# Kernel optimization log

Measured on AMD Instinct MI355X. Metric: run time of the kernel, lower is better.

## Reference

```python
import jax, jax.numpy as jnp
import numpy as np
import math

B, S, IN_DIM = 2048, 60, 211
D, H, L, DFF, NC = 192, 6, 3, 768, 35
DK = D // H


def make_pe(seq_len, d_model):
    pos = np.arange(seq_len)[:, None].astype(np.float32)
    div = np.exp(np.arange(0, d_model, 2).astype(np.float32) * (-math.log(10000.0) / d_model))
    pe = np.zeros((seq_len, d_model), dtype=np.float32)
    pe[:, 0::2] = np.sin(pos * div)
    pe[:, 1::2] = np.cos(pos * div)
    return jnp.asarray(pe)


def setup_inputs() -> dict:
    key = jax.random.key(0)
    ks = jax.random.split(key, 24)
    r = lambda k, shape, fan: jax.random.normal(k, shape, jnp.float32) * (1.0 / np.sqrt(fan))
    inp = {
        'x': jax.random.normal(ks[0], (B, S, IN_DIM), jnp.float32),
        'W_in': r(ks[1], (IN_DIM, D), IN_DIM), 'b_in': jnp.zeros((D,), jnp.float32),
        'pe': make_pe(S, D),
        'Wq': r(ks[2], (L, D, D), D), 'bq': jnp.zeros((L, D), jnp.float32),
        'Wk': r(ks[3], (L, D, D), D), 'bk': jnp.zeros((L, D), jnp.float32),
        'Wv': r(ks[4], (L, D, D), D), 'bv': jnp.zeros((L, D), jnp.float32),
        'Wo': r(ks[5], (L, D, D), D), 'bo': jnp.zeros((L, D), jnp.float32),
        'W1': r(ks[6], (L, D, DFF), D), 'b1': jnp.zeros((L, DFF), jnp.float32),
        'W2': r(ks[7], (L, DFF, D), DFF), 'b2': jnp.zeros((L, D), jnp.float32),
        'g1': jnp.ones((L, D), jnp.float32), 'be1': jnp.zeros((L, D), jnp.float32),
        'g2': jnp.ones((L, D), jnp.float32), 'be2': jnp.zeros((L, D), jnp.float32),
        'Wc1': r(ks[8], (D, D // 2), D), 'bc1': jnp.zeros((D // 2,), jnp.float32),
        'Wc2': r(ks[9], (D // 2, NC), D // 2), 'bc2': jnp.zeros((NC,), jnp.float32),
    }
    return inp


def layer_norm(x, g, b, eps=1e-5):
    mu = jnp.mean(x, axis=-1, keepdims=True)
    var = jnp.mean((x - mu) ** 2, axis=-1, keepdims=True)
    return (x - mu) * jax.lax.rsqrt(var + eps) * g + b


def mha(x, Wq, bq, Wk, bk, Wv, bv, Wo, bo):
    Bs, Ss, _ = x.shape
    q = (x @ Wq + bq).reshape(Bs, Ss, H, DK)
    k = (x @ Wk + bk).reshape(Bs, Ss, H, DK)
    v = (x @ Wv + bv).reshape(Bs, Ss, H, DK)
    scores = jnp.einsum('bqhd,bkhd->bhqk', q, k) / jnp.sqrt(jnp.float32(DK))
    attn = jax.nn.softmax(scores, axis=-1)
    ctx = jnp.einsum('bhqk,bkhd->bqhd', attn, v).reshape(Bs, Ss, D)
    return ctx @ Wo + bo


def encoder_layer(x, Wq, bq, Wk, bk, Wv, bv, Wo, bo, W1, b1, W2, b2, g1, be1, g2, be2):
    attn_out = mha(x, Wq, bq, Wk, bk, Wv, bv, Wo, bo)
    x = layer_norm(x + attn_out, g1, be1)
    ff = jax.nn.gelu(x @ W1 + b1, approximate=False) @ W2 + b2
    return layer_norm(x + ff, g2, be2)


def reference(x, W_in, b_in, pe, Wq, bq, Wk, bk, Wv, bv, Wo, bo,
              W1, b1, W2, b2, g1, be1, g2, be2, Wc1, bc1, Wc2, bc2):
    h = x @ W_in + b_in + pe  # [B,S,D]
    for l in range(L):
        h = encoder_layer(h, Wq[l], bq[l], Wk[l], bk[l], Wv[l], bv[l], Wo[l], bo[l],
                          W1[l], b1[l], W2[l], b2[l], g1[l], be1[l], g2[l], be2[l])
    hidden = jax.nn.gelu(h @ Wc1 + bc1, approximate=False)
    return hidden @ Wc2 + bc2  # [B,S,NC]
```

## Files before the change

kernel.cpp:

```cpp
#include <hip/hip_runtime.h>
#include <cmath>

#define B_   2048
#define S_   60
#define NTOK (B_*S_)
#define IND_ 211
#define D_   192
#define H_   6
#define DK_  32
#define L_   3
#define DFF_ 768
#define NC_  35
#define DH_  96

typedef unsigned short us_t;
typedef us_t us8 __attribute__((ext_vector_type(8)));
typedef us_t us4 __attribute__((ext_vector_type(4)));
typedef short sh8 __attribute__((ext_vector_type(8)));
typedef float f4 __attribute__((ext_vector_type(4)));

#define MFMA(a, b, cc) __builtin_amdgcn_mfma_f32_16x16x32_bf16((a), (b), (cc), 0, 0, 0)
#define ZACC(A, M, N) \
    for (int _i = 0; _i < (M); ++_i) \
        for (int _j = 0; _j < (N); ++_j) { \
            A[_i][_j][0] = 0.f; A[_i][_j][1] = 0.f; A[_i][_j][2] = 0.f; A[_i][_j][3] = 0.f; }
#define ZACC1(A, N) \
    for (int _j = 0; _j < (N); ++_j) { \
        A[_j][0] = 0.f; A[_j][1] = 0.f; A[_j][2] = 0.f; A[_j][3] = 0.f; }

__device__ __forceinline__ float bf2f(us_t u) {
    union { unsigned int i; float f; } v; v.i = ((unsigned int)u) << 16; return v.f;
}
__device__ __forceinline__ us_t f2bf(float f) {
    union { float f; unsigned int i; } v; v.f = f;
    unsigned int r = v.i + 0x7fffu + ((v.i >> 16) & 1u);
    return (us_t)(r >> 16);
}
__device__ __forceinline__ float gelu_f(float v) {
    float u = v * (0.7978845608f + 0.0356774081f * v * v);
    float e = __expf(2.f * u);
    float t = 1.f - 2.f / (e + 1.f);
    return 0.5f * v * (1.f + t);
}
__device__ __forceinline__ void gld16(const us_t* g, us_t* s) {
    __builtin_amdgcn_global_load_lds(
        (const __attribute__((address_space(1))) unsigned int*)(g),
        (__attribute__((address_space(3))) unsigned int*)(s), 16, 0, 0);
}

__global__ void prep_t(const float* __restrict__ in, us_t* __restrict__ out,
                       int K, int Kpad, int N)
{
    int e = blockIdx.x * 256 + threadIdx.x;
    if (e >= N * Kpad) return;
    int n = e / Kpad, kp = e % Kpad;
    out[e] = (kp < K) ? f2bf(in[(size_t)kp * N + n]) : (us_t)0;
}

__global__ void prep_ff(const float* __restrict__ W1, const float* __restrict__ W2,
                        us_t* __restrict__ W1T, us_t* __restrict__ W2T)
{
    int e = blockIdx.x * 256 + threadIdx.x;
    if (e >= L_ * 12 * 13824) return;
    int l = e / (12 * 13824), r = e % (12 * 13824);
    int tile = r / 13824, q = r % 13824;
    int col = q / 72, kk = q % 72;
    int cb = tile / 3, pc = tile % 3;
    us_t v1 = 0, v2 = 0;
    if (kk < 64) {
        v1 = f2bf(W1[((size_t)l * D_ + pc * 64 + kk) * DFF_ + cb * D_ + col]);
        v2 = f2bf(W2[((size_t)l * DFF_ + cb * D_ + pc * 64 + kk) * D_ + col]);
    }
    W1T[e] = v1; W2T[e] = v2;
}

__global__ __launch_bounds__(256) void inp_mfma(
    const float* __restrict__ x, const us_t* __restrict__ Wint,
    const float* __restrict__ b_in, const float* __restrict__ pe,
    us_t* __restrict__ h)
{
    __shared__ __align__(16) char smem[29696 + 27648];
    us_t* Xs = (us_t*)smem;
    us_t* Ws = (us_t*)(smem + 29696);
    const int tid = threadIdx.x;
    const int lane = tid & 63, wid = tid >> 6;
    const int g = lane >> 4, c = lane & 15;
    const int wr = wid >> 1, wc = wid & 1;
    const int row0 = blockIdx.x * 64;

    for (int e = tid; e < 64 * 224; e += 256) {
        int tok = e / 224, kp = e % 224;
        float v = (kp < IND_) ? x[(size_t)(row0 + tok) * IND_ + kp] : 0.f;
        Xs[tok * 232 + kp] = f2bf(v);
    }

    f4 acc[2][6];
    ZACC(acc, 2, 6);
    for (int pc = 0; pc < 4; ++pc) {
        __syncthreads();
        const int nk = (pc < 3) ? 64 : 32;
        const int per = nk / 8;
        for (int e = tid; e < 192 * per; e += 256) {
            int rw = e / per, v = e % per;
            *(us8*)&Ws[rw * 72 + v * 8] =
                *(const us8*)&Wint[(size_t)rw * 224 + pc * 64 + v * 8];
        }
        __syncthreads();
        for (int kk = 0; kk < nk / 32; ++kk) {
            const int ka = pc * 64 + kk * 32 + g * 8;
            const int kw = kk * 32 + g * 8;
            sh8 a0 = *(const sh8*)&Xs[(32 * wr + c) * 232 + ka];
            sh8 a1 = *(const sh8*)&Xs[(32 * wr + 16 + c) * 232 + ka];
            #pragma unroll
            for (int ni = 0; ni < 6; ++ni) {
                sh8 bf = *(const sh8*)&Ws[(96 * wc + 16 * ni + c) * 72 + kw];
                acc[0][ni] = MFMA(a0, bf, acc[0][ni]);
                acc[1][ni] = MFMA(a1, bf, acc[1][ni]);
            }
        }
    }
    #pragma unroll
    for (int ni = 0; ni < 6; ++ni) {
        const int col = 96 * wc + 16 * ni + c;
        const float bv = b_in[col];
        #pragma unroll
        for (int mi = 0; mi < 2; ++mi)
            #pragma unroll
            for (int r = 0; r < 4; ++r) {
                int tokg = row0 + 32 * wr + 16 * mi + 4 * g + r;
                int s = tokg % S_;
                float val = acc[mi][ni][r] + bv + pe[(size_t)s * D_ + col];
                h[(size_t)tokg * D_ + col] = f2bf(val);
            }
    }
}

__global__ __launch_bounds__(1024) void qkv_attn_wo(
    us_t* __restrict__ h,
    const us_t* __restrict__ Wqt, const us_t* __restrict__ Wkt,
    const us_t* __restrict__ Wvt, const us_t* __restrict__ Wot,
    const float* __restrict__ bq, const float* __restrict__ bk,
    const float* __restrict__ bv, const float* __restrict__ bo,
    const float* __restrict__ g1, const float* __restrict__ be1)
{
    __shared__ __align__(16) char smem[157696];
    us_t* Xs  = (us_t*)smem;
    us_t* Qs  = (us_t*)(smem + 25600);
    us_t* Ks  = (us_t*)(smem + 51200);
    us_t* Vt  = (us_t*)(smem + 76800);
    us_t* Ws  = (us_t*)(smem + 104448);
    us_t* Pb3 = (us_t*)(smem + 104448);
    us_t* Cx  = (us_t*)(smem + 132096);
    float* eL = (float*)(smem + 51200);

    const int tid = threadIdx.x;
    const int lane = tid & 63, wid = tid >> 6;
    const int g = lane >> 4, c = lane & 15;
    const int wr = wid >> 2, wc = wid & 3;
    us_t* hb = h + (size_t)blockIdx.x * (S_ * D_);

    for (int e = tid; e < 1536; e += 1024) {
        int tok = e / 24, v = e % 24;
        us8 u = {0, 0, 0, 0, 0, 0, 0, 0};
        if (tok < S_) u = *(const us8*)&hb[(size_t)tok * D_ + v * 8];
        *(us8*)&Xs[tok * 200 + v * 8] = u;
    }

    for (int m = 0; m < 3; ++m) {
        const us_t* Wt = (m == 0) ? Wqt : (m == 1) ? Wkt : Wvt;
        const float* bb = (m == 0) ? bq : (m == 1) ? bk : bv;
        f4 acc[3];
        ZACC1(acc, 3);
        for (int pc = 0; pc < 3; ++pc) {
            __syncthreads();
            for (int e = tid; e < 1536; e += 1024) {
                int rw = e >> 3, v = e & 7;
                *(us8*)&Ws[rw * 72 + v * 8] =
                    *(const us8*)&Wt[(size_t)rw * 192 + pc * 64 + v * 8];
            }
            __syncthreads();
            #pragma unroll
            for (int kk = 0; kk < 2; ++kk) {
                const int ka = pc * 64 + kk * 32 + g * 8;
                const int kw = kk * 32 + g * 8;
                sh8 a0 = *(const sh8*)&Xs[(16 * wr + c) * 200 + ka];
                #pragma unroll
                for (int ni = 0; ni < 3; ++ni) {
                    sh8 bf = *(const sh8*)&Ws[(48 * wc + 16 * ni + c) * 72 + kw];
                    acc[ni] = MFMA(a0, bf, acc[ni]);
                }
            }
        }
        #pragma unroll
        for (int ni = 0; ni < 3; ++ni) {
            const int col = 48 * wc + 16 * ni + c;
            const float bval = bb[col];
            #pragma unroll
            for (int r = 0; r < 4; ++r) {
                int tok = 16 * wr + 4 * g + r;
                us_t o = f2bf(acc[ni][r] + bval);
                if (m == 0)      Qs[tok * 200 + col] = o;
                else if (m == 1) Ks[tok * 200 + col] = o;
                else             Vt[col * 72 + tok] = o;
            }
        }
    }
    __syncthreads();

    for (int rr2 = 0; rr2 < 2; ++rr2) {
        const bool act = (wid < 12);
        const int hh = 3 * rr2 + (wid >> 2);
        const int hgrp = wid & 3;
        us_t* Pb = Pb3 + (size_t)(wid >> 2) * 4608;
        if (act) {
            f4 sc[4];
            ZACC1(sc, 4);
            const int ka = 32 * hh + g * 8;
            sh8 aq = *(const sh8*)&Qs[(16 * hgrp + c) * 200 + ka];
            #pragma unroll
            for (int ni = 0; ni < 4; ++ni) {
                sh8 bk8 = *(const sh8*)&Ks[(16 * ni + c) * 200 + ka];
                sc[ni] = MFMA(aq, bk8, sc[ni]);
            }
            #pragma unroll
            for (int r = 0; r < 4; ++r) {
                float mx = -1e30f;
                #pragma unroll
                for (int ni = 0; ni < 4; ++ni) {
                    float v = sc[ni][r] * 0.17677669529663687f;
                    if (16 * ni + c >= S_) v = -1e30f;
                    sc[ni][r] = v;
                    mx = fmaxf(mx, v);
                }
                mx = fmaxf(mx, __shfl_xor(mx, 1));
                mx = fmaxf(mx, __shfl_xor(mx, 2));
                mx = fmaxf(mx, __shfl_xor(mx, 4));
                mx = fmaxf(mx, __shfl_xor(mx, 8));
                float sum = 0.f;
                #pragma unroll
                for (int ni = 0; ni < 4; ++ni) {
                    float e = __expf(sc[ni][r] - mx);
                    sc[ni][r] = e; sum += e;
                }
                sum += __shfl_xor(sum, 1);
                sum += __shfl_xor(sum, 2);
                sum += __shfl_xor(sum, 4);
                sum += __shfl_xor(sum, 8);
                const float inv = 1.f / sum;
                #pragma unroll
                for (int ni = 0; ni < 4; ++ni)
                    Pb[(16 * hgrp + 4 * g + r) * 72 + 16 * ni + c] = f2bf(sc[ni][r] * inv);
            }
        }
        __syncthreads();
        if (act) {
            f4 ov[2];
            ZACC1(ov, 2);
            #pragma unroll
            for (int kk = 0; kk < 2; ++kk) {
                sh8 ap = *(const sh8*)&Pb[(16 * hgrp + c) * 72 + kk * 32 + g * 8];
                #pragma unroll
                for (int n2 = 0; n2 < 2; ++n2) {
                    sh8 bv8 = *(const sh8*)&Vt[(32 * hh + 16 * n2 + c) * 72 + kk * 32 + g * 8];
                    ov[n2] = MFMA(ap, bv8, ov[n2]);
                }
            }
            #pragma unroll
            for (int n2 = 0; n2 < 2; ++n2)
                #pragma unroll
                for (int r = 0; r < 4; ++r)
                    Cx[(16 * hgrp + 4 * g + r) * 200 + 32 * hh + 16 * n2 + c] = f2bf(ov[n2][r]);
        }
        __syncthreads();
    }

    f4 aw[3];
    ZACC1(aw, 3);
    for (int pc = 0; pc < 3; ++pc) {
        __syncthreads();
        for (int e = tid; e < 1536; e += 1024) {
            int rw = e >> 3, v = e & 7;
            *(us8*)&Ws[rw * 72 + v * 8] =
                *(const us8*)&Wot[(size_t)rw * 192 + pc * 64 + v * 8];
        }
        __syncthreads();
        #pragma unroll
        for (int kk = 0; kk < 2; ++kk) {
            const int ka = pc * 64 + kk * 32 + g * 8;
            const int kw = kk * 32 + g * 8;
            sh8 a0 = *(const sh8*)&Cx[(16 * wr + c) * 200 + ka];
            #pragma unroll
            for (int ni = 0; ni < 3; ++ni) {
                sh8 bf = *(const sh8*)&Ws[(48 * wc + 16 * ni + c) * 72 + kw];
                aw[ni] = MFMA(a0, bf, aw[ni]);
            }
        }
    }
    __syncthreads();
    #pragma unroll
    for (int ni = 0; ni < 3; ++ni) {
        const int col = 48 * wc + 16 * ni + c;
        const float bov = bo[col];
        #pragma unroll
        for (int r = 0; r < 4; ++r) {
            int tok = 16 * wr + 4 * g + r;
            eL[tok * 200 + col] = aw[ni][r] + bov + bf2f(Xs[tok * 200 + col]);
        }
    }
    __syncthreads();
    {
        const int tl = tid >> 4, t16 = tid & 15;
        float vals[12], sum = 0.f, ssq = 0.f;
        #pragma unroll
        for (int jv = 0; jv < 3; ++jv) {
            float4 v4 = *(const float4*)&eL[tl * 200 + t16 * 12 + jv * 4];
            vals[jv*4+0] = v4.x; vals[jv*4+1] = v4.y; vals[jv*4+2] = v4.z; vals[jv*4+3] = v4.w;
            sum += v4.x + v4.y + v4.z + v4.w;
            ssq += v4.x*v4.x + v4.y*v4.y + v4.z*v4.z + v4.w*v4.w;
        }
        sum += __shfl_xor(sum, 1); sum += __shfl_xor(sum, 2);
        sum += __shfl_xor(sum, 4); sum += __shfl_xor(sum, 8);
        ssq += __shfl_xor(ssq, 1); ssq += __shfl_xor(ssq, 2);
        ssq += __shfl_xor(ssq, 4); ssq += __shfl_xor(ssq, 8);
        const float mean = sum * (1.f / D_);
        const float var  = ssq * (1.f / D_) - mean * mean;
        const float rstd = rsqrtf(var + 1e-5f);
        if (tl < S_) {
            #pragma unroll
            for (int jv = 0; jv < 3; ++jv) {
                us4 o4;
                #pragma unroll
                for (int j = 0; j < 4; ++j) {
                    int col = t16 * 12 + jv * 4 + j;
                    o4[j] = f2bf((vals[jv*4+j] - mean) * rstd * g1[col] + be1[col]);
                }
                *(us4*)&hb[(size_t)tl * D_ + t16 * 12 + jv * 4] = o4;
            }
        }
    }
}

__global__ __launch_bounds__(1024) void ff_mfma(
    us_t* __restrict__ hio,
    const us_t* __restrict__ W1T, const float* __restrict__ b1,
    const us_t* __restrict__ W2T, const float* __restrict__ b2,
    const float* __restrict__ gamma, const float* __restrict__ beta)
{
    __shared__ __align__(16) char smem[157696];
    us_t* Xs  = (us_t*)smem;
    us_t* Ts  = (us_t*)(smem + 51200);
    us_t* Wsb = (us_t*)(smem + 102400);
    float* eL = (float*)(smem + 51200);

    const int tid = threadIdx.x;
    const int lane = tid & 63, wid = tid >> 6;
    const int g = lane >> 4, c = lane & 15;
    const int wr = wid >> 2, wc = wid & 3;
    const int row0 = blockIdx.x * 128;

    auto stageW = [&](int t) {
        const int cb2 = t / 6, ph = (t % 6) / 3, pc2 = t % 3;
        const us_t* src = (ph ? W2T : W1T) + (size_t)(cb2 * 3 + pc2) * 13824;
        us_t* dst = Wsb + (size_t)(t & 1) * 13824;
        for (int i = wid; i < 27; i += 16)
            gld16(src + i * 512 + lane * 8, dst + i * 512);
    };

    for (int e = tid; e < 3072; e += 1024) {
        int tok = e / 24, v = e % 24;
        *(us8*)&Xs[tok * 200 + v * 8] = *(const us8*)&hio[(size_t)(row0 + tok) * D_ + v * 8];
    }
    stageW(0);
    __syncthreads();

    f4 acc2[2][3];
    ZACC(acc2, 2, 3);
    for (int cb = 0; cb < 4; ++cb) {
        f4 acc1[2][3];
        ZACC(acc1, 2, 3);
        #pragma unroll
        for (int pc = 0; pc < 3; ++pc) {
            const int t = cb * 6 + pc;
            if (t < 23) stageW(t + 1);
            const us_t* W = Wsb + (size_t)(t & 1) * 13824;
            #pragma unroll
            for (int kk = 0; kk < 2; ++kk) {
                const int ka = pc * 64 + kk * 32 + g * 8;
                const int kw = kk * 32 + g * 8;
                sh8 a0 = *(const sh8*)&Xs[(32 * wr + c) * 200 + ka];
                sh8 a1 = *(const sh8*)&Xs[(32 * wr + 16 + c) * 200 + ka];
                #pragma unroll
                for (int ni = 0; ni < 3; ++ni) {
                    sh8 bf = *(const sh8*)&W[(48 * wc + 16 * ni + c) * 72 + kw];
                    acc1[0][ni] = MFMA(a0, bf, acc1[0][ni]);
                    acc1[1][ni] = MFMA(a1, bf, acc1[1][ni]);
                }
            }
            if (pc == 2) {
                #pragma unroll
                for (int ni = 0; ni < 3; ++ni) {
                    const int col = 48 * wc + 16 * ni + c;
                    const float b1v = b1[cb * 192 + col];
                    #pragma unroll
                    for (int mi = 0; mi < 2; ++mi)
                        #pragma unroll
                        for (int r = 0; r < 4; ++r) {
                            int tok = 32 * wr + 16 * mi + 4 * g + r;
                            Ts[tok * 200 + col] = f2bf(gelu_f(acc1[mi][ni][r] + b1v));
                        }
                }
            }
            __syncthreads();
        }
        #pragma unroll
        for (int pc = 0; pc < 3; ++pc) {
            const int t = cb * 6 + 3 + pc;
            if (t < 23) stageW(t + 1);
            const us_t* W = Wsb + (size_t)(t & 1) * 13824;
            #pragma unroll
            for (int kk = 0; kk < 2; ++kk) {
                const int ka = pc * 64 + kk * 32 + g * 8;
                const int kw = kk * 32 + g * 8;
                sh8 a0 = *(const sh8*)&Ts[(32 * wr + c) * 200 + ka];
                sh8 a1 = *(const sh8*)&Ts[(32 * wr + 16 + c) * 200 + ka];
                #pragma unroll
                for (int ni = 0; ni < 3; ++ni) {
                    sh8 bf = *(const sh8*)&W[(48 * wc + 16 * ni + c) * 72 + kw];
                    acc2[0][ni] = MFMA(a0, bf, acc2[0][ni]);
                    acc2[1][ni] = MFMA(a1, bf, acc2[1][ni]);
                }
            }
            __syncthreads();
        }
    }

    for (int p = 0; p < 2; ++p) {
        if (p) __syncthreads();
        if ((wr >> 1) == p) {
            #pragma unroll
            for (int ni = 0; ni < 3; ++ni) {
                const int col = 48 * wc + 16 * ni + c;
                const float b2v = b2[col];
                #pragma unroll
                for (int mi = 0; mi < 2; ++mi)
                    #pragma unroll
                    for (int r = 0; r < 4; ++r) {
                        int tok = 32 * wr + 16 * mi + 4 * g + r;
                        eL[(tok - 64 * p) * 200 + col] =
                            acc2[mi][ni][r] + b2v + bf2f(Xs[tok * 200 + col]);
                    }
            }
        }
        __syncthreads();
        {
            const int tl = tid >> 4, t16 = tid & 15;
            float vals[12], sum = 0.f, ssq = 0.f;
            #pragma unroll
            for (int jv = 0; jv < 3; ++jv) {
                float4 v4 = *(const float4*)&eL[tl * 200 + t16 * 12 + jv * 4];
                vals[jv*4+0] = v4.x; vals[jv*4+1] = v4.y;
                vals[jv*4+2] = v4.z; vals[jv*4+3] = v4.w;
                sum += v4.x + v4.y + v4.z + v4.w;
                ssq += v4.x*v4.x + v4.y*v4.y + v4.z*v4.z + v4.w*v4.w;
            }
            sum += __shfl_xor(sum, 1); sum += __shfl_xor(sum, 2);
            sum += __shfl_xor(sum, 4); sum += __shfl_xor(sum, 8);
            ssq += __shfl_xor(ssq, 1); ssq += __shfl_xor(ssq, 2);
            ssq += __shfl_xor(ssq, 4); ssq += __shfl_xor(ssq, 8);
            const float mean = sum * (1.f / D_);
            const float var  = ssq * (1.f / D_) - mean * mean;
            const float rstd = rsqrtf(var + 1e-5f);
            #pragma unroll
            for (int jv = 0; jv < 3; ++jv) {
                us4 o4;
                #pragma unroll
                for (int j = 0; j < 4; ++j) {
                    int col = t16 * 12 + jv * 4 + j;
                    o4[j] = f2bf((vals[jv*4+j] - mean) * rstd * gamma[col] + beta[col]);
                }
                *(us4*)&hio[(size_t)(row0 + 64 * p + tl) * D_ + t16 * 12 + jv * 4] = o4;
            }
        }
    }
}

__global__ __launch_bounds__(256) void clf1_mfma(
    const us_t* __restrict__ h, const us_t* __restrict__ Wc1t,
    const float* __restrict__ bc1, us_t* __restrict__ hid)
{
    __shared__ __align__(16) char smem[25600 + 13824];
    us_t* Xs = (us_t*)smem;
    us_t* Ws = (us_t*)(smem + 25600);
    const int tid = threadIdx.x;
    const int lane = tid & 63, wid = tid >> 6;
    const int g = lane >> 4, c = lane & 15;
    const int wr = wid >> 1, wc = wid & 1;
    const int row0 = blockIdx.x * 64;

    for (int e = tid; e < 1536; e += 256) {
        int tok = e / 24, v = e % 24;
        *(us8*)&Xs[tok * 200 + v * 8] = *(const us8*)&h[(size_t)(row0 + tok) * D_ + v * 8];
    }
    f4 acc[2][3];
    ZACC(acc, 2, 3);
    for (int pc = 0; pc < 3; ++pc) {
        __syncthreads();
        for (int e = tid; e < 768; e += 256) {
            int rw = e >> 3, v = e & 7;
            *(us8*)&Ws[rw * 72 + v * 8] =
                *(const us8*)&Wc1t[(size_t)rw * 192 + pc * 64 + v * 8];
        }
        __syncthreads();
        #pragma unroll
        for (int kk = 0; kk < 2; ++kk) {
            const int ka = pc * 64 + kk * 32 + g * 8;
            const int kw = kk * 32 + g * 8;
            sh8 a0 = *(const sh8*)&Xs[(32 * wr + c) * 200 + ka];
            sh8 a1 = *(const sh8*)&Xs[(32 * wr + 16 + c) * 200 + ka];
            #pragma unroll
            for (int ni = 0; ni < 3; ++ni) {
                sh8 bf = *(const sh8*)&Ws[(48 * wc + 16 * ni + c) * 72 + kw];
                acc[0][ni] = MFMA(a0, bf, acc[0][ni]);
                acc[1][ni] = MFMA(a1, bf, acc[1][ni]);
            }
        }
    }
    #pragma unroll
    for (int ni = 0; ni < 3; ++ni) {
        const int col = 48 * wc + 16 * ni + c;
        const float bv = bc1[col];
        #pragma unroll
        for (int mi = 0; mi < 2; ++mi)
            #pragma unroll
            for (int r = 0; r < 4; ++r) {
                int tok = row0 + 32 * wr + 16 * mi + 4 * g + r;
                hid[(size_t)tok * DH_ + col] = f2bf(gelu_f(acc[mi][ni][r] + bv));
            }
    }
}

__global__ __launch_bounds__(256) void clf2_kernel(
    const us_t* __restrict__ hid, const float* __restrict__ Wc2,
    const float* __restrict__ bc2, float* __restrict__ out)
{
    __shared__ us_t Hs[64 * 104];
    __shared__ float Wl[DH_ * NC_];
    __shared__ float bl[NC_];
    const int tid = threadIdx.x;
    const int row0 = blockIdx.x * 64;
    for (int e = tid; e < 768; e += 256) {
        int tok = e / 12, v = e % 12;
        *(us8*)&Hs[tok * 104 + v * 8] = *(const us8*)&hid[(size_t)(row0 + tok) * DH_ + v * 8];
    }
    for (int e = tid; e < DH_ * NC_; e += 256) Wl[e] = Wc2[e];
    if (tid < NC_) bl[tid] = bc2[tid];
    __syncthreads();
    for (int e = tid; e < 64 * NC_; e += 256) {
        const int tok = e / NC_, col = e % NC_;
        float acc = bl[col];
        #pragma unroll 8
        for (int kk = 0; kk < DH_; ++kk)
            acc = fmaf(bf2f(Hs[tok * 104 + kk]), Wl[kk * NC_ + col], acc);
        out[(size_t)(row0 + tok) * NC_ + col] = acc;
    }
}

extern "C" void kernel_launch(void* const* d_in, const int* in_sizes, int n_in,
                              void* d_out, int out_size, void* d_ws, size_t ws_size,
                              hipStream_t stream)
{
    const float* x    = (const float*)d_in[0];
    const float* W_in = (const float*)d_in[1];
    const float* b_in = (const float*)d_in[2];
    const float* pe   = (const float*)d_in[3];
    const float* Wq   = (const float*)d_in[4];
    const float* bq   = (const float*)d_in[5];
    const float* Wk   = (const float*)d_in[6];
    const float* bk   = (const float*)d_in[7];
    const float* Wv   = (const float*)d_in[8];
    const float* bv   = (const float*)d_in[9];
    const float* Wo   = (const float*)d_in[10];
    const float* bo   = (const float*)d_in[11];
    const float* W1   = (const float*)d_in[12];
    const float* b1   = (const float*)d_in[13];
    const float* W2   = (const float*)d_in[14];
    const float* b2   = (const float*)d_in[15];
    const float* g1   = (const float*)d_in[16];
    const float* be1  = (const float*)d_in[17];
    const float* g2   = (const float*)d_in[18];
    const float* be2  = (const float*)d_in[19];
    const float* Wc1  = (const float*)d_in[20];
    const float* bc1  = (const float*)d_in[21];
    const float* Wc2  = (const float*)d_in[22];
    const float* bc2  = (const float*)d_in[23];
    float* outp = (float*)d_out;

    us_t* h    = (us_t*)d_ws;
    us_t* hid  = h + (size_t)NTOK * D_;
    us_t* Wint = hid + (size_t)NTOK * DH_;
    us_t* Wqt  = Wint + 192 * 224;
    us_t* Wkt  = Wqt + 3 * 36864;
    us_t* Wvt  = Wkt + 3 * 36864;
    us_t* Wot  = Wvt + 3 * 36864;
    us_t* W1T  = Wot + 3 * 36864;
    us_t* W2T  = W1T + (size_t)L_ * 12 * 13824;
    us_t* Wc1t = W2T + (size_t)L_ * 12 * 13824;

    prep_t<<<168, 256, 0, stream>>>(W_in, Wint, IND_, 224, D_);
    for (int l = 0; l < L_; ++l) {
        prep_t<<<144, 256, 0, stream>>>(Wq + (size_t)l * 36864, Wqt + (size_t)l * 36864, 192, 192, 192);
        prep_t<<<144, 256, 0, stream>>>(Wk + (size_t)l * 36864, Wkt + (size_t)l * 36864, 192, 192, 192);
        prep_t<<<144, 256, 0, stream>>>(Wv + (size_t)l * 36864, Wvt + (size_t)l * 36864, 192, 192, 192);
        prep_t<<<144, 256, 0, stream>>>(Wo + (size_t)l * 36864, Wot + (size_t)l * 36864, 192, 192, 192);
    }
    prep_ff<<<(L_ * 12 * 13824 + 255) / 256, 256, 0, stream>>>(W1, W2, W1T, W2T);
    prep_t<<<72, 256, 0, stream>>>(Wc1, Wc1t, 192, 192, DH_);

    inp_mfma<<<NTOK / 64, 256, 0, stream>>>(x, Wint, b_in, pe, h);

    for (int l = 0; l < L_; ++l) {
        qkv_attn_wo<<<B_, 1024, 0, stream>>>(
            h,
            Wqt + (size_t)l * 36864, Wkt + (size_t)l * 36864,
            Wvt + (size_t)l * 36864, Wot + (size_t)l * 36864,
            bq + l * D_, bk + l * D_, bv + l * D_, bo + l * D_,
            g1 + l * D_, be1 + l * D_);
        ff_mfma<<<NTOK / 128, 1024, 0, stream>>>(
            h, W1T + (size_t)l * 12 * 13824, b1 + l * DFF_,
            W2T + (size_t)l * 12 * 13824, b2 + l * D_,
            g2 + l * D_, be2 + l * D_);
    }

    clf1_mfma<<<NTOK / 64, 256, 0, stream>>>(h, Wc1t, bc1, hid);
    clf2_kernel<<<NTOK / 64, 256, 0, stream>>>(hid, Wc2, bc2, outp);
}
```

Before: 1.180 ms.

## Double-buffer attention weight tiles via async LDS loads and fuse classifier kernels

Weights for Q/K/V/O are pre-tiled into one padded layout, so the attention kernel can prefetch the next 64-column slice with global_load_lds into a double buffer while the MFMAs consume the current one. This replaces the synchronous per-slice copy and removes one barrier per step. Attention now computes all six heads' probabilities before any context product, which cuts barriers but needs more shared memory (Cx now reuses the Q region). The two classifier kernels are fused so the hidden activations stay in LDS, and the many weight-prep launches are merged into fewer kernels.

```diff
diff --git a/kernel.cpp b/kernel.cpp
--- a/kernel.cpp
+++ b/kernel.cpp
@@ -48,13 +48,38 @@
         (__attribute__((address_space(3))) unsigned int*)(s), 16, 0, 0);
 }
 
-__global__ void prep_t(const float* __restrict__ in, us_t* __restrict__ out,
-                       int K, int Kpad, int N)
+__global__ void prep_misc(const float* __restrict__ W_in, const float* __restrict__ Wc1,
+                          us_t* __restrict__ Wint, us_t* __restrict__ Wc1t)
 {
     int e = blockIdx.x * 256 + threadIdx.x;
-    if (e >= N * Kpad) return;
-    int n = e / Kpad, kp = e % Kpad;
-    out[e] = (kp < K) ? f2bf(in[(size_t)kp * N + n]) : (us_t)0;
+    const int n1 = 192 * 224, n2 = 96 * 192;
+    if (e < n1) {
+        int n = e / 224, kp = e % 224;
+        Wint[e] = (kp < IND_) ? f2bf(W_in[(size_t)kp * D_ + n]) : (us_t)0;
+    } else if (e < n1 + n2) {
+        int r = e - n1;
+        int n = r / 192, kp = r % 192;
+        Wc1t[r] = f2bf(Wc1[(size_t)kp * DH_ + n]);
+    }
+}
+
+__global__ void prep_qkvw(const float* __restrict__ Wq, const float* __restrict__ Wk,
+                          const float* __restrict__ Wv, const float* __restrict__ Wo,
+                          us_t* __restrict__ WI)
+{
+    int e = blockIdx.x * 256 + threadIdx.x;
+    if (e >= L_ * 12 * 13824) return;
+    int l = e / (12 * 13824), r = e % (12 * 13824);
+    int t = r / 13824, q = r % 13824;
+    int rw = q / 72, kk = q % 72;
+    us_t v = 0;
+    if (kk < 64) {
+        int mat = (t < 9) ? (t / 3) : 3;
+        int pc  = (t < 9) ? (t % 3) : (t - 9);
+        const float* W = (mat == 0) ? Wq : (mat == 1) ? Wk : (mat == 2) ? Wv : Wo;
+        v = f2bf(W[(size_t)l * 36864 + (size_t)(pc * 64 + kk) * D_ + rw]);
+    }
+    WI[e] = v;
 }
 
 __global__ void prep_ff(const float* __restrict__ W1, const float* __restrict__ W2,
@@ -136,21 +161,19 @@
 }
 
 __global__ __launch_bounds__(1024) void qkv_attn_wo(
-    us_t* __restrict__ h,
-    const us_t* __restrict__ Wqt, const us_t* __restrict__ Wkt,
-    const us_t* __restrict__ Wvt, const us_t* __restrict__ Wot,
+    us_t* __restrict__ h, const us_t* __restrict__ WI,
     const float* __restrict__ bq, const float* __restrict__ bk,
     const float* __restrict__ bv, const float* __restrict__ bo,
     const float* __restrict__ g1, const float* __restrict__ be1)
 {
-    __shared__ __align__(16) char smem[157696];
+    __shared__ __align__(16) char smem[159744];
     us_t* Xs  = (us_t*)smem;
     us_t* Qs  = (us_t*)(smem + 25600);
     us_t* Ks  = (us_t*)(smem + 51200);
     us_t* Vt  = (us_t*)(smem + 76800);
-    us_t* Ws  = (us_t*)(smem + 104448);
-    us_t* Pb3 = (us_t*)(smem + 104448);
-    us_t* Cx  = (us_t*)(smem + 132096);
+    us_t* Wsb = (us_t*)(smem + 104448);
+    us_t* P6  = (us_t*)(smem + 104448);
+    us_t* Cx  = (us_t*)(smem + 25600);
     float* eL = (float*)(smem + 51200);
 
     const int tid = threadIdx.x;
@@ -159,26 +182,30 @@
     const int wr = wid >> 2, wc = wid & 3;
     us_t* hb = h + (size_t)blockIdx.x * (S_ * D_);
 
+    auto stageI = [&](int t) {
+        const us_t* src = WI + (size_t)t * 13824;
+        us_t* dst = Wsb + (size_t)(t & 1) * 13824;
+        for (int i = wid; i < 27; i += 16)
+            gld16(src + i * 512 + lane * 8, dst + i * 512);
+    };
+
     for (int e = tid; e < 1536; e += 1024) {
         int tok = e / 24, v = e % 24;
         us8 u = {0, 0, 0, 0, 0, 0, 0, 0};
         if (tok < S_) u = *(const us8*)&hb[(size_t)tok * D_ + v * 8];
         *(us8*)&Xs[tok * 200 + v * 8] = u;
     }
+    stageI(0);
+    __syncthreads();
 
     for (int m = 0; m < 3; ++m) {
-        const us_t* Wt = (m == 0) ? Wqt : (m == 1) ? Wkt : Wvt;
         const float* bb = (m == 0) ? bq : (m == 1) ? bk : bv;
         f4 acc[3];
         ZACC1(acc, 3);
         for (int pc = 0; pc < 3; ++pc) {
-            __syncthreads();
-            for (int e = tid; e < 1536; e += 1024) {
-                int rw = e >> 3, v = e & 7;
-                *(us8*)&Ws[rw * 72 + v * 8] =
-                    *(const us8*)&Wt[(size_t)rw * 192 + pc * 64 + v * 8];
-            }
-            __syncthreads();
+            const int t = m * 3 + pc;
+            if (t < 8) stageI(t + 1);
+            const us_t* W = Wsb + (size_t)(t & 1) * 13824;
             #pragma unroll
             for (int kk = 0; kk < 2; ++kk) {
                 const int ka = pc * 64 + kk * 32 + g * 8;
@@ -186,10 +213,11 @@
                 sh8 a0 = *(const sh8*)&Xs[(16 * wr + c) * 200 + ka];
                 #pragma unroll
                 for (int ni = 0; ni < 3; ++ni) {
-                    sh8 bf = *(const sh8*)&Ws[(48 * wc + 16 * ni + c) * 72 + kw];
+                    sh8 bf = *(const sh8*)&W[(48 * wc + 16 * ni + c) * 72 + kw];
                     acc[ni] = MFMA(a0, bf, acc[ni]);
                 }
             }
+            __syncthreads();
         }
         #pragma unroll
         for (int ni = 0; ni < 3; ++ni) {
@@ -207,12 +235,11 @@
     }
     __syncthreads();
 
-    for (int rr2 = 0; rr2 < 2; ++rr2) {
-        const bool act = (wid < 12);
-        const int hh = 3 * rr2 + (wid >> 2);
-        const int hgrp = wid & 3;
-        us_t* Pb = Pb3 + (size_t)(wid >> 2) * 4608;
-        if (act) {
+    for (int r2 = 0; r2 < 2; ++r2) {
+        if (wid < 12) {
+            const int hh = 3 * r2 + (wid >> 2);
+            const int hgrp = wid & 3;
+            us_t* Pb = P6 + (size_t)hh * 4608;
             f4 sc[4];
             ZACC1(sc, 4);
             const int ka = 32 * hh + g * 8;
@@ -252,8 +279,14 @@
                     Pb[(16 * hgrp + 4 * g + r) * 72 + 16 * ni + c] = f2bf(sc[ni][r] * inv);
             }
         }
-        __syncthreads();
-        if (act) {
+    }
+    __syncthreads();
+
+    for (int r2 = 0; r2 < 2; ++r2) {
+        if (wid < 12) {
+            const int hh = 3 * r2 + (wid >> 2);
+            const int hgrp = wid & 3;
+            const us_t* Pb = P6 + (size_t)hh * 4608;
             f4 ov[2];
             ZACC1(ov, 2);
             #pragma unroll
@@ -271,19 +304,17 @@
                 for (int r = 0; r < 4; ++r)
                     Cx[(16 * hgrp + 4 * g + r) * 200 + 32 * hh + 16 * n2 + c] = f2bf(ov[n2][r]);
         }
-        __syncthreads();
-    }
-
+    }
+    __syncthreads();
+
+    stageI(9);
+    __syncthreads();
     f4 aw[3];
     ZACC1(aw, 3);
     for (int pc = 0; pc < 3; ++pc) {
-        __syncthreads();
-        for (int e = tid; e < 1536; e += 1024) {
-            int rw = e >> 3, v = e & 7;
-            *(us8*)&Ws[rw * 72 + v * 8] =
-                *(const us8*)&Wot[(size_t)rw * 192 + pc * 64 + v * 8];
-        }
-        __syncthreads();
+        const int t = 9 + pc;
+        if (pc < 2) stageI(t + 1);
+        const us_t* W = Wsb + (size_t)(t & 1) * 13824;
         #pragma unroll
         for (int kk = 0; kk < 2; ++kk) {
             const int ka = pc * 64 + kk * 32 + g * 8;
@@ -291,12 +322,12 @@
             sh8 a0 = *(const sh8*)&Cx[(16 * wr + c) * 200 + ka];
             #pragma unroll
             for (int ni = 0; ni < 3; ++ni) {
-                sh8 bf = *(const sh8*)&Ws[(48 * wc + 16 * ni + c) * 72 + kw];
+                sh8 bf = *(const sh8*)&W[(48 * wc + 16 * ni + c) * 72 + kw];
                 aw[ni] = MFMA(a0, bf, aw[ni]);
             }
         }
-    }
-    __syncthreads();
+        __syncthreads();
+    }
     #pragma unroll
     for (int ni = 0; ni < 3; ++ni) {
         const int col = 48 * wc + 16 * ni + c;
@@ -484,13 +515,17 @@
     }
 }
 
-__global__ __launch_bounds__(256) void clf1_mfma(
+__global__ __launch_bounds__(256) void clf12(
     const us_t* __restrict__ h, const us_t* __restrict__ Wc1t,
-    const float* __restrict__ bc1, us_t* __restrict__ hid)
-{
-    __shared__ __align__(16) char smem[25600 + 13824];
+    const float* __restrict__ bc1, const float* __restrict__ Wc2,
+    const float* __restrict__ bc2, float* __restrict__ out)
+{
+    __shared__ __align__(16) char smem[25600 + 13824 + 13312];
     us_t* Xs = (us_t*)smem;
     us_t* Ws = (us_t*)(smem + 25600);
+    us_t* Hs = (us_t*)(smem + 25600 + 13824);
+    __shared__ float Wl[DH_ * NC_];
+    __shared__ float bl[NC_];
     const int tid = threadIdx.x;
     const int lane = tid & 63, wid = tid >> 6;
     const int g = lane >> 4, c = lane & 15;
@@ -501,6 +536,9 @@
         int tok = e / 24, v = e % 24;
         *(us8*)&Xs[tok * 200 + v * 8] = *(const us8*)&h[(size_t)(row0 + tok) * D_ + v * 8];
     }
+    for (int e = tid; e < DH_ * NC_; e += 256) Wl[e] = Wc2[e];
+    if (tid < NC_) bl[tid] = bc2[tid];
+
     f4 acc[2][3];
     ZACC(acc, 2, 3);
     for (int pc = 0; pc < 3; ++pc) {
@@ -533,35 +571,18 @@
         for (int mi = 0; mi < 2; ++mi)
             #pragma unroll
             for (int r = 0; r < 4; ++r) {
-                int tok = row0 + 32 * wr + 16 * mi + 4 * g + r;
-                hid[(size_t)tok * DH_ + col] = f2bf(gelu_f(acc[mi][ni][r] + bv));
-            }
-    }
-}
-
-__global__ __launch_bounds__(256) void clf2_kernel(
-    const us_t* __restrict__ hid, const float* __restrict__ Wc2,
-    const float* __restrict__ bc2, float* __restrict__ out)
-{
-    __shared__ us_t Hs[64 * 104];
-    __shared__ float Wl[DH_ * NC_];
-    __shared__ float bl[NC_];
-    const int tid = threadIdx.x;
-    const int row0 = blockIdx.x * 64;
-    for (int e = tid; e < 768; e += 256) {
-        int tok = e / 12, v = e % 12;
-        *(us8*)&Hs[tok * 104 + v * 8] = *(const us8*)&hid[(size_t)(row0 + tok) * DH_ + v * 8];
-    }
-    for (int e = tid; e < DH_ * NC_; e += 256) Wl[e] = Wc2[e];
-    if (tid < NC_) bl[tid] = bc2[tid];
+                int tok = 32 * wr + 16 * mi + 4 * g + r;
+                Hs[tok * 104 + col] = f2bf(gelu_f(acc[mi][ni][r] + bv));
+            }
+    }
     __syncthreads();
     for (int e = tid; e < 64 * NC_; e += 256) {
         const int tok = e / NC_, col = e % NC_;
-        float acc = bl[col];
+        float a = bl[col];
         #pragma unroll 8
         for (int kk = 0; kk < DH_; ++kk)
-            acc = fmaf(bf2f(Hs[tok * 104 + kk]), Wl[kk * NC_ + col], acc);
-        out[(size_t)(row0 + tok) * NC_ + col] = acc;
+            a = fmaf(bf2f(Hs[tok * 104 + kk]), Wl[kk * NC_ + col], a);
+        out[(size_t)(row0 + tok) * NC_ + col] = a;
     }
 }
 
@@ -596,33 +617,21 @@
     float* outp = (float*)d_out;
 
     us_t* h    = (us_t*)d_ws;
-    us_t* hid  = h + (size_t)NTOK * D_;
-    us_t* Wint = hid + (size_t)NTOK * DH_;
-    us_t* Wqt  = Wint + 192 * 224;
-    us_t* Wkt  = Wqt + 3 * 36864;
-    us_t* Wvt  = Wkt + 3 * 36864;
-    us_t* Wot  = Wvt + 3 * 36864;
-    us_t* W1T  = Wot + 3 * 36864;
+    us_t* Wint = h + (size_t)NTOK * D_;
+    us_t* WIq  = Wint + 192 * 224;
+    us_t* W1T  = WIq + (size_t)L_ * 12 * 13824;
     us_t* W2T  = W1T + (size_t)L_ * 12 * 13824;
     us_t* Wc1t = W2T + (size_t)L_ * 12 * 13824;
 
-    prep_t<<<168, 256, 0, stream>>>(W_in, Wint, IND_, 224, D_);
-    for (int l = 0; l < L_; ++l) {
-        prep_t<<<144, 256, 0, stream>>>(Wq + (size_t)l * 36864, Wqt + (size_t)l * 36864, 192, 192, 192);
-        prep_t<<<144, 256, 0, stream>>>(Wk + (size_t)l * 36864, Wkt + (size_t)l * 36864, 192, 192, 192);
-        prep_t<<<144, 256, 0, stream>>>(Wv + (size_t)l * 36864, Wvt + (size_t)l * 36864, 192, 192, 192);
-        prep_t<<<144, 256, 0, stream>>>(Wo + (size_t)l * 36864, Wot + (size_t)l * 36864, 192, 192, 192);
-    }
+    prep_misc<<<(192 * 224 + 96 * 192 + 255) / 256, 256, 0, stream>>>(W_in, Wc1, Wint, Wc1t);
+    prep_qkvw<<<(L_ * 12 * 13824 + 255) / 256, 256, 0, stream>>>(Wq, Wk, Wv, Wo, WIq);
     prep_ff<<<(L_ * 12 * 13824 + 255) / 256, 256, 0, stream>>>(W1, W2, W1T, W2T);
-    prep_t<<<72, 256, 0, stream>>>(Wc1, Wc1t, 192, 192, DH_);
 
     inp_mfma<<<NTOK / 64, 256, 0, stream>>>(x, Wint, b_in, pe, h);
 
     for (int l = 0; l < L_; ++l) {
         qkv_attn_wo<<<B_, 1024, 0, stream>>>(
-            h,
-            Wqt + (size_t)l * 36864, Wkt + (size_t)l * 36864,
-            Wvt + (size_t)l * 36864, Wot + (size_t)l * 36864,
+            h, WIq + (size_t)l * 12 * 13824,
             bq + l * D_, bk + l * D_, bv + l * D_, bo + l * D_,
             g1 + l * D_, be1 + l * D_);
         ff_mfma<<<NTOK / 128, 1024, 0, stream>>>(
@@ -631,6 +640,5 @@
             g2 + l * D_, be2 + l * D_);
     }
 
-    clf1_mfma<<<NTOK / 64, 256, 0, stream>>>(h, Wc1t, bc1, hid);
-    clf2_kernel<<<NTOK / 64, 256, 0, stream>>>(hid, Wc2, bc2, outp);
-}
+    clf12<<<NTOK / 64, 256, 0, stream>>>(h, Wc1t, bc1, Wc2, bc2, outp);
+}
```

After: 1.109 ms (median of 2 runs). 6.0% less time.
